# Kernel tuning notes

Measured on AMD Instinct MI355X. Metric: run time of the kernel, lower is better.

Reference implementation:

```python
import jax, jax.numpy as jnp
import numpy as np

EMBED_DIM = 1024
NUM_HEADS = 16
HEAD_DIM = EMBED_DIM // NUM_HEADS


def setup_inputs() -> dict:
    key = jax.random.key(0)
    ks = jax.random.split(key, 9)
    B, T, C = 2, 2048, EMBED_DIM
    s = 1.0 / np.sqrt(C)
    return {
        "x": jax.random.normal(ks[0], (B, T, C), dtype=jnp.float32),
        "Wq": jax.random.normal(ks[1], (C, C), dtype=jnp.float32) * s,
        "bq": jnp.zeros((C,), dtype=jnp.float32),
        "Wk": jax.random.normal(ks[2], (C, C), dtype=jnp.float32) * s,
        "bk": jnp.zeros((C,), dtype=jnp.float32),
        "Wv": jax.random.normal(ks[3], (C, C), dtype=jnp.float32) * s,
        "bv": jnp.zeros((C,), dtype=jnp.float32),
        "Wo": jax.random.normal(ks[4], (C, C), dtype=jnp.float32) * s,
        "bo": jnp.zeros((C,), dtype=jnp.float32),
    }


def reference(x, Wq, bq, Wk, bk, Wv, bv, Wo, bo):
    B, T, C = x.shape
    H, D = NUM_HEADS, HEAD_DIM
    # projections (torch Linear: x @ W.T + b; here W stored as [in,out])
    q = (x @ Wq + bq).reshape(B, T, H, D).transpose(0, 2, 1, 3)  # [B,H,T,D]
    k = (x @ Wk + bk).reshape(B, T, H, D).transpose(0, 2, 1, 3)
    v = (x @ Wv + bv).reshape(B, T, H, D).transpose(0, 2, 1, 3)
    scores = jnp.einsum("bhtd,bhsd->bhts", q, k) / jnp.sqrt(jnp.float32(D))
    causal = jnp.tril(jnp.ones((T, T), dtype=bool))  # keep lower triangle
    scores = jnp.where(causal, scores, -jnp.inf)
    weights = jax.nn.softmax(scores, axis=-1)
    attended = jnp.einsum("bhts,bhsd->bhtd", weights, v)
    attended = attended.transpose(0, 2, 1, 3).reshape(B, T, C)
    return attended @ Wo + bo
```

## Files before the change

kernel.cpp:

```cpp
#include <hip/hip_runtime.h>
#include <math.h>


#define BLOCK 256

typedef __attribute__((ext_vector_type(8))) short bf16x8;
typedef __attribute__((ext_vector_type(4))) float f32x4;
typedef __attribute__((ext_vector_type(16))) float f32x16;

__device__ inline short f2bf(float f) {
  union { float f; unsigned u; } c; c.f = f;
  unsigned u = c.u;
  unsigned r = (u + 0x7fffu + ((u >> 16) & 1u)) >> 16;
  return (short)r;
}


__global__ void cvt_all_kernel(const float* __restrict__ x,
                               const float* __restrict__ Wq, const float* __restrict__ Wk,
                               const float* __restrict__ Wv, const float* __restrict__ Wo,
                               short* __restrict__ xb,
                               short* __restrict__ Wtqkv, short* __restrict__ Wto) {
  __shared__ float tile[32][33];
  __shared__ __align__(16) short xtile[4096];
  int z = blockIdx.z;
  if (z >= 4) {
    int blk = blockIdx.x + (blockIdx.y << 5);
    int rt = blk >> 2, sq = blk & 3;
    int row_l = threadIdx.x >> 4, q = threadIdx.x & 15;
    const float* xr = x + (size_t)(rt * 16 + row_l) * 1024 + sq * 256 + q * 16;
    float4 f0 = *(const float4*)(xr);
    float4 f1 = *(const float4*)(xr + 4);
    float4 f2 = *(const float4*)(xr + 8);
    float4 f3 = *(const float4*)(xr + 12);
    alignas(16) short e0[8], e1[8];
    e0[0] = f2bf(f0.x); e0[1] = f2bf(f0.y); e0[2] = f2bf(f0.z); e0[3] = f2bf(f0.w);
    e0[4] = f2bf(f1.x); e0[5] = f2bf(f1.y); e0[6] = f2bf(f1.z); e0[7] = f2bf(f1.w);
    e1[0] = f2bf(f2.x); e1[1] = f2bf(f2.y); e1[2] = f2bf(f2.z); e1[3] = f2bf(f2.w);
    e1[4] = f2bf(f3.x); e1[5] = f2bf(f3.y); e1[6] = f2bf(f3.z); e1[7] = f2bf(f3.w);
    int c0 = q * 2, c1 = q * 2 + 1;
    *(int4*)&xtile[(c0 * 16 + (row_l ^ (c0 & 15))) * 8] = *(const int4*)e0;
    *(int4*)&xtile[(c1 * 16 + (row_l ^ (c1 & 15))) * 8] = *(const int4*)e1;
    __syncthreads();
    int lc = threadIdx.x & 15, c8x = threadIdx.x >> 4;
#pragma unroll
    for (int hh = 0; hh < 2; hh++) {
      int c8l = c8x + hh * 16;
      int4 v = *(const int4*)&xtile[(c8l * 16 + (lc ^ (c8l & 15))) * 8];
      int s = sq * 4 + (c8l >> 3), c8 = c8l & 7;
      *(int4*)&xb[(size_t)rt * 16384 + s * 1024 + c8 * 128 + lc * 8] = v;
    }
    return;
  }
  const float* W = (z == 0) ? Wq : (z == 1) ? Wk : (z == 2) ? Wv : Wo;
  short* outp = (z == 3) ? Wto : (Wtqkv + (size_t)z * 1024 * 1024);
  int k0 = blockIdx.x * 32, n0 = blockIdx.y * 32;
  int tr = threadIdx.x >> 5, tc = threadIdx.x & 31;
#pragma unroll
  for (int i = 0; i < 4; i++)
    tile[tr + i * 8][tc] = W[(k0 + tr + i * 8) * 1024 + n0 + tc];
  __syncthreads();
#pragma unroll
  for (int i = 0; i < 4; i++)
    outp[(n0 + tr + i * 8) * 1024 + k0 + tc] = f2bf(tile[tc][tr + i * 8]);
}


__global__ __launch_bounds__(BLOCK, 3) void gemm_qkv_kernel(
    const short* __restrict__ A, const short* __restrict__ Wt,
    const float* __restrict__ bq, const float* __restrict__ bk,
    const float* __restrict__ bv,
    short* __restrict__ Qo, short* __restrict__ Ko, short* __restrict__ Vo) {
  const int Kd = 1024;
  const float QSCL = 0.18033688011f;
  int p = blockIdx.x;
  int xcd = p & 7, j = p >> 3;
  int m0 = ((xcd & 3) * 8 + (j & 7)) * 128;
  int n0 = ((xcd >> 2) * 12 + (j >> 3)) * 128;
  int t = threadIdx.x;
  int lane = t & 63, wv = t >> 6;
  int quad = lane >> 4, lc = lane & 15;
  int wy = wv >> 1, wx = wv & 1;
  __shared__ short Bs[128 * 64];
  f32x4 acc[4][4] = {};

  int sr = wv * 32 + (lane >> 3);
  int schk = lane & 7;
  const short* Bb = Wt + (size_t)(n0 + sr) * Kd + schk * 8;
  int wslot = schk ^ (lane >> 3);
  short* wb = &Bs[sr * 64 + wslot * 8];
  const short* Ap = A + (size_t)m0 * 1024;
  int abase = wy * 4 * 16384 + lane * 8;

  bf16x8 sB[4];
#pragma unroll
  for (int i = 0; i < 4; i++)
    sB[i] = *(const bf16x8*)(Bb + (size_t)(i * 8) * Kd);

  int rx = lc & 7;
  for (int step = 0; step < 16; step++) {
#pragma unroll
    for (int i = 0; i < 4; i++)
      *(bf16x8*)(wb + i * 8 * 64) = sB[i];
    asm volatile("s_waitcnt lgkmcnt(0)" ::: "memory");
    __builtin_amdgcn_s_barrier();
    asm volatile("" ::: "memory");
    bf16x8 af2[2][4];
#pragma unroll
    for (int kc2 = 0; kc2 < 2; kc2++)
#pragma unroll
      for (int i = 0; i < 4; i++)
        af2[kc2][i] = *(const bf16x8*)(Ap + (size_t)abase + i * 16384 +
                                       step * 1024 + kc2 * 512);
    if (step + 1 < 16) {
      int koff = (step + 1) * 64;
#pragma unroll
      for (int i = 0; i < 4; i++)
        sB[i] = *(const bf16x8*)(Bb + (size_t)(i * 8) * Kd + koff);
    }
#pragma unroll
    for (int kc = 0; kc < 2; kc++) {
      bf16x8 bf[4];
#pragma unroll
      for (int i = 0; i < 4; i++)
        bf[i] = *(const bf16x8*)&Bs[(wx * 64 + i * 16 + lc) * 64 +
                                    ((kc * 4 + quad) ^ rx) * 8];
#pragma unroll
      for (int mi = 0; mi < 4; mi++)
#pragma unroll
        for (int ni = 0; ni < 4; ni++)
          acc[mi][ni] = __builtin_amdgcn_mfma_f32_16x16x32_bf16(af2[kc][mi], bf[ni], acc[mi][ni], 0, 0, 0);
    }
    asm volatile("s_waitcnt lgkmcnt(0)" ::: "memory");
    __builtin_amdgcn_s_barrier();
    asm volatile("" ::: "memory");
  }
#pragma unroll
  for (int mi = 0; mi < 4; mi++) {
    int row = m0 + wy * 64 + mi * 16 + quad * 4;
#pragma unroll
    for (int ni = 0; ni < 4; ni++) {
      int col = n0 + wx * 64 + ni * 16 + lc;
      int which = col >> 10;
      int hd = col & 1023;
      int h = hd >> 6, d = hd & 63;
      float bb = (which == 0) ? bq[hd] : (which == 1) ? bk[hd] : bv[hd];
      if (which == 2) {
        alignas(8) short pk[4];
#pragma unroll
        for (int r = 0; r < 4; r++) pk[r] = f2bf(acc[mi][ni][r] + bb);
        int b = row >> 11, tt = row & 2047;
        *(int2*)&Vo[((size_t)(b * 16 + h) * 64 + d) * 2048 + tt] = *(const int2*)pk;
      } else {
#pragma unroll
        for (int r = 0; r < 4; r++) {
          int rw = row + r;
          int b = rw >> 11, tt = rw & 2047;
          float val = acc[mi][ni][r] + bb;
          if (which == 0) {
            Qo[((size_t)(b * 16 + h) * 2048 + tt) * 64 + d] = f2bf(val * QSCL);
          } else {
            Ko[((size_t)(b * 16 + h) * 2048 + tt) * 64 + d] = f2bf(val);
          }
        }
      }
    }
  }
}


__global__ __launch_bounds__(BLOCK) void gemm_out_kernel(
    const short* __restrict__ A, const short* __restrict__ Wt,
    const float* __restrict__ bias, float* __restrict__ Out) {
  const int Kd = 1024;
  int m0 = blockIdx.x * 64, n0 = blockIdx.y * 128;
  int t = threadIdx.x;
  int lane = t & 63, wv = t >> 6;
  int quad = lane >> 4, lc = lane & 15;
  int wy = wv >> 1, wx = wv & 1;
  __shared__ short As[64 * 64];
  __shared__ short Bs[128 * 64];
  f32x4 acc[2][4] = {};

  int lr = lane >> 3;
  int schk = lane & 7;
  int wslot = schk ^ lr;
  int srA = wv * 16 + lr;
  int srB = wv * 32 + lr;
  const short* Ab = A + (size_t)(m0 + srA) * Kd + schk * 8;
  const short* Bb = Wt + (size_t)(n0 + srB) * Kd + schk * 8;
  short* wa = &As[srA * 64 + wslot * 8];
  short* wb = &Bs[srB * 64 + wslot * 8];

  bf16x8 sA[2], sB[4];
#pragma unroll
  for (int i = 0; i < 2; i++) sA[i] = *(const bf16x8*)(Ab + (size_t)(i * 8) * Kd);
#pragma unroll
  for (int i = 0; i < 4; i++) sB[i] = *(const bf16x8*)(Bb + (size_t)(i * 8) * Kd);

  int rx = lc & 7;
  for (int step = 0; step < 16; step++) {
#pragma unroll
    for (int i = 0; i < 2; i++) *(bf16x8*)(wa + i * 8 * 64) = sA[i];
#pragma unroll
    for (int i = 0; i < 4; i++) *(bf16x8*)(wb + i * 8 * 64) = sB[i];
    asm volatile("s_waitcnt lgkmcnt(0)" ::: "memory");
    __builtin_amdgcn_s_barrier();
    asm volatile("" ::: "memory");
    if (step + 1 < 16) {
      int koff = (step + 1) * 64;
#pragma unroll
      for (int i = 0; i < 2; i++)
        sA[i] = *(const bf16x8*)(Ab + (size_t)(i * 8) * Kd + koff);
#pragma unroll
      for (int i = 0; i < 4; i++)
        sB[i] = *(const bf16x8*)(Bb + (size_t)(i * 8) * Kd + koff);
    }
#pragma unroll
    for (int kc = 0; kc < 2; kc++) {
      bf16x8 af[2], bf[4];
#pragma unroll
      for (int i = 0; i < 2; i++)
        af[i] = *(const bf16x8*)&As[(wy * 32 + i * 16 + lc) * 64 +
                                    ((kc * 4 + quad) ^ rx) * 8];
#pragma unroll
      for (int i = 0; i < 4; i++)
        bf[i] = *(const bf16x8*)&Bs[(wx * 64 + i * 16 + lc) * 64 +
                                    ((kc * 4 + quad) ^ rx) * 8];
#pragma unroll
      for (int mi = 0; mi < 2; mi++)
#pragma unroll
        for (int ni = 0; ni < 4; ni++)
          acc[mi][ni] = __builtin_amdgcn_mfma_f32_16x16x32_bf16(af[mi], bf[ni], acc[mi][ni], 0, 0, 0);
    }
    asm volatile("s_waitcnt lgkmcnt(0)" ::: "memory");
    __builtin_amdgcn_s_barrier();
    asm volatile("" ::: "memory");
  }
#pragma unroll
  for (int mi = 0; mi < 2; mi++) {
    int row = m0 + wy * 32 + mi * 16 + quad * 4;
#pragma unroll
    for (int ni = 0; ni < 4; ni++) {
      int col = n0 + wx * 64 + ni * 16 + lc;
      float bb = bias[col];
#pragma unroll
      for (int r = 0; r < 4; r++)
        Out[(size_t)(row + r) * 1024 + col] = acc[mi][ni][r] + bb;
    }
  }
}


__global__ __launch_bounds__(BLOCK, 2) void attn_kernel(
    const short* __restrict__ Q, const short* __restrict__ K,
    const short* __restrict__ Vt, short* __restrict__ Oa) {
  int p = blockIdx.x;
  int bh = ((p & 7) << 2) | ((p >> 3) & 3);
  int pair = p >> 5;
  int t = threadIdx.x;
  int lane = t & 63, w = t >> 6;
  int qh = w & 1, kh = w >> 1;
  int ln = lane & 31, lh = lane >> 5;
  const short* Qb = Q + (size_t)bh * 2048 * 64;
  const short* Kb = K + (size_t)bh * 2048 * 64;
  const short* Vg = Vt + (size_t)bh * 64 * 2048;
  int b = bh >> 4, h = bh & 15;

  __shared__ short Kt[64 * 64];
  __shared__ short Vs[64 * 64];
  __shared__ __align__(16) short Ps[4][32 * 72];
  __shared__ float lx[2][64];
  short* Pw = Ps[w];

  int srow = t >> 3;
  int schk = t & 7;
  int wslot = (schk ^ (srow & 7)) * 8;
  const float M2 = 14.5f;
  int xk = ln & 7;

  for (int sp = 0; sp < 2; sp++) {
    int s = sp ? (31 - pair) : pair;
    int q0 = s * 64;
    int q0w = q0 + qh * 32;
    int qmaxw = q0w + 31;
    int ntiles = s + 1;

    bf16x8 qf[4];
#pragma unroll
    for (int c = 0; c < 4; c++)
      qf[c] = *(const bf16x8*)&Qb[(size_t)(q0w + ln) * 64 + c * 16 + lh * 8];

    f32x16 O0 = {}, O1 = {};
    float lsum = 0.f;

    bf16x8 sK[2], sV[2];
#pragma unroll
    for (int i = 0; i < 2; i++) {
      int r = i * 32 + srow;
      sK[i] = *(const bf16x8*)&Kb[(size_t)r * 64 + schk * 8];
      sV[i] = *(const bf16x8*)&Vg[(size_t)r * 2048 + schk * 8];
    }
    for (int kt = 0; kt < ntiles; kt++) {
#pragma unroll
      for (int i = 0; i < 2; i++) {
        int r = i * 32 + srow;
        *(bf16x8*)&Kt[r * 64 + wslot] = sK[i];
        *(bf16x8*)&Vs[r * 64 + wslot] = sV[i];
      }
      asm volatile("s_waitcnt lgkmcnt(0)" ::: "memory");
      __builtin_amdgcn_s_barrier();
      asm volatile("" ::: "memory");
      if (kt + 1 < ntiles) {
        int kb2 = (kt + 1) * 64;
#pragma unroll
        for (int i = 0; i < 2; i++) {
          int r = i * 32 + srow;
          sK[i] = *(const bf16x8*)&Kb[(size_t)(kb2 + r) * 64 + schk * 8];
          sV[i] = *(const bf16x8*)&Vg[(size_t)r * 2048 + kb2 + schk * 8];
        }
      }
      int grpbase = kt * 64 + kh * 32;
      if (grpbase <= qmaxw) {
        f32x16 S = {};
#pragma unroll
        for (int c = 0; c < 4; c++) {
          int ch = c * 2 + lh;
          bf16x8 kf = *(const bf16x8*)&Kt[(kh * 32 + ln) * 64 + (ch ^ xk) * 8];
          S = __builtin_amdgcn_mfma_f32_32x32x16_bf16(kf, qf[c], S, 0, 0, 0);
        }
        if (kt == ntiles - 1) {
          int qg = q0w + ln;
#pragma unroll
          for (int reg = 0; reg < 16; reg++) {
            int key = grpbase + (reg & 3) + 8 * (reg >> 2) + 4 * lh;
            if (key > qg) S[reg] = -3.0e38f;
          }
        }
#pragma unroll
        for (int g = 0; g < 4; g++) {
          unsigned u[4];
#pragma unroll
          for (int i = 0; i < 4; i++) {
            union { float f; unsigned v; } cc;
            cc.f = __builtin_amdgcn_exp2f(S[g * 4 + i] - M2);
            lsum += cc.f;
            u[i] = cc.v + 0x8000u;
          }
          int2 pk;
          pk.x = (int)__builtin_amdgcn_perm(u[1], u[0], 0x07060302);
          pk.y = (int)__builtin_amdgcn_perm(u[3], u[2], 0x07060302);
          *(int2*)&Pw[ln * 72 + g * 8 + lh * 4] = pk;
        }
#pragma unroll
        for (int c2 = 0; c2 < 2; c2++) {
          bf16x8 pf = *(const bf16x8*)&Pw[ln * 72 + c2 * 16 + lh * 8];
          int ch = kh * 4 + c2 * 2 + lh;
          bf16x8 v0 = *(const bf16x8*)&Vs[ln * 64 + (ch ^ xk) * 8];
          bf16x8 v1 = *(const bf16x8*)&Vs[(32 + ln) * 64 + (ch ^ xk) * 8];
          O0 = __builtin_amdgcn_mfma_f32_32x32x16_bf16(v0, pf, O0, 0, 0, 0);
          O1 = __builtin_amdgcn_mfma_f32_32x32x16_bf16(v1, pf, O1, 0, 0, 0);
        }
      }
      asm volatile("s_waitcnt lgkmcnt(0)" ::: "memory");
      __builtin_amdgcn_s_barrier();
      asm volatile("" ::: "memory");
    }

    float* ob = (float*)&Ps[0][0];
    if (kh == 1) {
      float* obw = ob + qh * 2048;
#pragma unroll
      for (int dh = 0; dh < 2; dh++)
#pragma unroll
        for (int reg = 0; reg < 16; reg++)
          obw[((dh * 16 + reg) * 2 + lh) * 32 + ln] = dh ? O1[reg] : O0[reg];
      lx[qh][lane] = lsum;
    }
    __syncthreads();
    if (kh == 0) {
      float* obw = ob + qh * 2048;
#pragma unroll
      for (int reg = 0; reg < 16; reg++) {
        O0[reg] += obw[((0 * 16 + reg) * 2 + lh) * 32 + ln];
        O1[reg] += obw[((1 * 16 + reg) * 2 + lh) * 32 + ln];
      }
      float lt = lsum + lx[qh][lane];
      lt += __shfl_xor(lt, 32, 64);
      float inv = 1.0f / lt;
      size_t rowbase = (size_t)(b * 2048 + q0w + ln) * 1024 + h * 64;
#pragma unroll
      for (int dh = 0; dh < 2; dh++)
#pragma unroll
        for (int g = 0; g < 4; g++) {
          alignas(8) short pk[4];
#pragma unroll
          for (int i = 0; i < 4; i++) {
            float v = dh ? O1[g * 4 + i] : O0[g * 4 + i];
            pk[i] = f2bf(v * inv);
          }
          *(int2*)&Oa[rowbase + dh * 32 + g * 8 + lh * 4] = *(const int2*)pk;
        }
    }
  }
}


extern "C" void kernel_launch(void* const* d_in, const int* in_sizes, int n_in,
                              void* d_out, int out_size, void* d_ws, size_t ws_size,
                              hipStream_t stream) {
  const float* x = (const float*)d_in[0];
  const float* Wq = (const float*)d_in[1];
  const float* bq = (const float*)d_in[2];
  const float* Wk = (const float*)d_in[3];
  const float* bk = (const float*)d_in[4];
  const float* Wv = (const float*)d_in[5];
  const float* bv = (const float*)d_in[6];
  const float* Wo = (const float*)d_in[7];
  const float* bo = (const float*)d_in[8];
  char* ws = (char*)d_ws;
  const size_t MB = 1024 * 1024;
  short* xb = (short*)(ws);
  short* Wtqkv = (short*)(ws + 8 * MB);
  short* Wto = (short*)(ws + 14 * MB);
  short* Qb = (short*)(ws + 17 * MB);
  short* Kb = (short*)(ws + 25 * MB);
  short* Vb = (short*)(ws + 33 * MB);
  short* Att = (short*)(ws + 41 * MB);
  float* out = (float*)d_out;

  cvt_all_kernel<<<dim3(32, 32, 5), BLOCK, 0, stream>>>(x, Wq, Wk, Wv, Wo, xb, Wtqkv, Wto);
  gemm_qkv_kernel<<<dim3(768), BLOCK, 0, stream>>>(xb, Wtqkv, bq, bk, bv, Qb, Kb, Vb);
  attn_kernel<<<512, BLOCK, 0, stream>>>(Qb, Kb, Vb, Att);
  gemm_out_kernel<<<dim3(64, 8), BLOCK, 0, stream>>>(Att, Wto, bo, out);
}
```

Before: 175.1 us.

## Assign each wave its own 32 query rows over 128-row blocks, drop key-split reduction

The attention kernel previously had each block handle two 64-row query tiles (a balanced pair). Within a tile, waves split the key dimension in halves and merged partial outputs through shared memory. Now each block handles one 128-row query tile, with the 16 tiles assigned largest-first. Each of the four waves owns 32 query rows and walks all keys itself, which removes the cross-wave O/lsum reduction and its extra barrier. In exchange, per-block work is unbalanced across the grid, and waves with early query rows sit idle on later key tiles because of the causal mask.

Result: slower. 179.7 us (+2.6%).

```diff
diff --git a/kernel.cpp b/kernel.cpp
--- a/kernel.cpp
+++ b/kernel.cpp
@@ -257,10 +257,10 @@
     const short* __restrict__ Vt, short* __restrict__ Oa) {
   int p = blockIdx.x;
   int bh = ((p & 7) << 2) | ((p >> 3) & 3);
-  int pair = p >> 5;
+  int g = p >> 5;
+  int s = (g < 8) ? (15 - g) : (g - 8);
   int t = threadIdx.x;
   int lane = t & 63, w = t >> 6;
-  int qh = w & 1, kh = w >> 1;
   int ln = lane & 31, lh = lane >> 5;
   const short* Qb = Q + (size_t)bh * 2048 * 64;
   const short* Kb = K + (size_t)bh * 2048 * 64;
@@ -270,7 +270,6 @@
   __shared__ short Kt[64 * 64];
   __shared__ short Vs[64 * 64];
   __shared__ __align__(16) short Ps[4][32 * 72];
-  __shared__ float lx[2][64];
   short* Pw = Ps[w];
 
   int srow = t >> 3;
@@ -279,57 +278,56 @@
   const float M2 = 14.5f;
   int xk = ln & 7;
 
-  for (int sp = 0; sp < 2; sp++) {
-    int s = sp ? (31 - pair) : pair;
-    int q0 = s * 64;
-    int q0w = q0 + qh * 32;
-    int qmaxw = q0w + 31;
-    int ntiles = s + 1;
-
-    bf16x8 qf[4];
-#pragma unroll
-    for (int c = 0; c < 4; c++)
-      qf[c] = *(const bf16x8*)&Qb[(size_t)(q0w + ln) * 64 + c * 16 + lh * 8];
-
-    f32x16 O0 = {}, O1 = {};
-    float lsum = 0.f;
-
-    bf16x8 sK[2], sV[2];
+  int q0w = s * 128 + w * 32;
+  int qmaxw = q0w + 31;
+  int ntiles = 2 * (s + 1);
+
+  bf16x8 qf[4];
+#pragma unroll
+  for (int c = 0; c < 4; c++)
+    qf[c] = *(const bf16x8*)&Qb[(size_t)(q0w + ln) * 64 + c * 16 + lh * 8];
+
+  f32x16 O0 = {}, O1 = {};
+  float lsum = 0.f;
+
+  bf16x8 sK[2], sV[2];
+#pragma unroll
+  for (int i = 0; i < 2; i++) {
+    int r = i * 32 + srow;
+    sK[i] = *(const bf16x8*)&Kb[(size_t)r * 64 + schk * 8];
+    sV[i] = *(const bf16x8*)&Vg[(size_t)r * 2048 + schk * 8];
+  }
+  for (int kt = 0; kt < ntiles; kt++) {
 #pragma unroll
     for (int i = 0; i < 2; i++) {
       int r = i * 32 + srow;
-      sK[i] = *(const bf16x8*)&Kb[(size_t)r * 64 + schk * 8];
-      sV[i] = *(const bf16x8*)&Vg[(size_t)r * 2048 + schk * 8];
-    }
-    for (int kt = 0; kt < ntiles; kt++) {
+      *(bf16x8*)&Kt[r * 64 + wslot] = sK[i];
+      *(bf16x8*)&Vs[r * 64 + wslot] = sV[i];
+    }
+    asm volatile("s_waitcnt lgkmcnt(0)" ::: "memory");
+    __builtin_amdgcn_s_barrier();
+    asm volatile("" ::: "memory");
+    if (kt + 1 < ntiles) {
+      int kb2 = (kt + 1) * 64;
 #pragma unroll
       for (int i = 0; i < 2; i++) {
         int r = i * 32 + srow;
-        *(bf16x8*)&Kt[r * 64 + wslot] = sK[i];
-        *(bf16x8*)&Vs[r * 64 + wslot] = sV[i];
+        sK[i] = *(const bf16x8*)&Kb[(size_t)(kb2 + r) * 64 + schk * 8];
+        sV[i] = *(const bf16x8*)&Vg[(size_t)r * 2048 + kb2 + schk * 8];
       }
-      asm volatile("s_waitcnt lgkmcnt(0)" ::: "memory");
-      __builtin_amdgcn_s_barrier();
-      asm volatile("" ::: "memory");
-      if (kt + 1 < ntiles) {
-        int kb2 = (kt + 1) * 64;
-#pragma unroll
-        for (int i = 0; i < 2; i++) {
-          int r = i * 32 + srow;
-          sK[i] = *(const bf16x8*)&Kb[(size_t)(kb2 + r) * 64 + schk * 8];
-          sV[i] = *(const bf16x8*)&Vg[(size_t)r * 2048 + kb2 + schk * 8];
-        }
-      }
-      int grpbase = kt * 64 + kh * 32;
+    }
+#pragma unroll
+    for (int kg = 0; kg < 2; kg++) {
+      int grpbase = kt * 64 + kg * 32;
       if (grpbase <= qmaxw) {
         f32x16 S = {};
 #pragma unroll
         for (int c = 0; c < 4; c++) {
           int ch = c * 2 + lh;
-          bf16x8 kf = *(const bf16x8*)&Kt[(kh * 32 + ln) * 64 + (ch ^ xk) * 8];
+          bf16x8 kf = *(const bf16x8*)&Kt[(kg * 32 + ln) * 64 + (ch ^ xk) * 8];
           S = __builtin_amdgcn_mfma_f32_32x32x16_bf16(kf, qf[c], S, 0, 0, 0);
         }
-        if (kt == ntiles - 1) {
+        if (grpbase + 31 > q0w) {
           int qg = q0w + ln;
 #pragma unroll
           for (int reg = 0; reg < 16; reg++) {
@@ -338,71 +336,54 @@
           }
         }
 #pragma unroll
-        for (int g = 0; g < 4; g++) {
+        for (int g4 = 0; g4 < 4; g4++) {
           unsigned u[4];
+          float e[4];
 #pragma unroll
           for (int i = 0; i < 4; i++) {
             union { float f; unsigned v; } cc;
-            cc.f = __builtin_amdgcn_exp2f(S[g * 4 + i] - M2);
-            lsum += cc.f;
+            cc.f = __builtin_amdgcn_exp2f(S[g4 * 4 + i] - M2);
+            e[i] = cc.f;
             u[i] = cc.v + 0x8000u;
           }
+          lsum += (e[0] + e[1]) + (e[2] + e[3]);
           int2 pk;
           pk.x = (int)__builtin_amdgcn_perm(u[1], u[0], 0x07060302);
           pk.y = (int)__builtin_amdgcn_perm(u[3], u[2], 0x07060302);
-          *(int2*)&Pw[ln * 72 + g * 8 + lh * 4] = pk;
+          *(int2*)&Pw[ln * 72 + kg * 32 + g4 * 8 + lh * 4] = pk;
         }
 #pragma unroll
-        for (int c2 = 0; c2 < 2; c2++) {
-          bf16x8 pf = *(const bf16x8*)&Pw[ln * 72 + c2 * 16 + lh * 8];
-          int ch = kh * 4 + c2 * 2 + lh;
+        for (int cc = 0; cc < 2; cc++) {
+          bf16x8 pf = *(const bf16x8*)&Pw[ln * 72 + kg * 32 + cc * 16 + lh * 8];
+          int ch = kg * 4 + cc * 2 + lh;
           bf16x8 v0 = *(const bf16x8*)&Vs[ln * 64 + (ch ^ xk) * 8];
           bf16x8 v1 = *(const bf16x8*)&Vs[(32 + ln) * 64 + (ch ^ xk) * 8];
           O0 = __builtin_amdgcn_mfma_f32_32x32x16_bf16(v0, pf, O0, 0, 0, 0);
           O1 = __builtin_amdgcn_mfma_f32_32x32x16_bf16(v1, pf, O1, 0, 0, 0);
         }
       }
-      asm volatile("s_waitcnt lgkmcnt(0)" ::: "memory");
-      __builtin_amdgcn_s_barrier();
-      asm volatile("" ::: "memory");
-    }
-
-    float* ob = (float*)&Ps[0][0];
-    if (kh == 1) {
-      float* obw = ob + qh * 2048;
-#pragma unroll
-      for (int dh = 0; dh < 2; dh++)
-#pragma unroll
-        for (int reg = 0; reg < 16; reg++)
-          obw[((dh * 16 + reg) * 2 + lh) * 32 + ln] = dh ? O1[reg] : O0[reg];
-      lx[qh][lane] = lsum;
-    }
-    __syncthreads();
-    if (kh == 0) {
-      float* obw = ob + qh * 2048;
-#pragma unroll
-      for (int reg = 0; reg < 16; reg++) {
-        O0[reg] += obw[((0 * 16 + reg) * 2 + lh) * 32 + ln];
-        O1[reg] += obw[((1 * 16 + reg) * 2 + lh) * 32 + ln];
+    }
+    asm volatile("s_waitcnt lgkmcnt(0)" ::: "memory");
+    __builtin_amdgcn_s_barrier();
+    asm volatile("" ::: "memory");
+  }
+
+  float lt = lsum;
+  lt += __shfl_xor(lt, 32, 64);
+  float inv = 1.0f / lt;
+  size_t rowbase = (size_t)(b * 2048 + q0w + ln) * 1024 + h * 64;
+#pragma unroll
+  for (int dh = 0; dh < 2; dh++)
+#pragma unroll
+    for (int g4 = 0; g4 < 4; g4++) {
+      alignas(8) short pk[4];
+#pragma unroll
+      for (int i = 0; i < 4; i++) {
+        float v = dh ? O1[g4 * 4 + i] : O0[g4 * 4 + i];
+        pk[i] = f2bf(v * inv);
       }
-      float lt = lsum + lx[qh][lane];
-      lt += __shfl_xor(lt, 32, 64);
-      float inv = 1.0f / lt;
-      size_t rowbase = (size_t)(b * 2048 + q0w + ln) * 1024 + h * 64;
-#pragma unroll
-      for (int dh = 0; dh < 2; dh++)
-#pragma unroll
-        for (int g = 0; g < 4; g++) {
-          alignas(8) short pk[4];
-#pragma unroll
-          for (int i = 0; i < 4; i++) {
-            float v = dh ? O1[g * 4 + i] : O0[g * 4 + i];
-            pk[i] = f2bf(v * inv);
-          }
-          *(int2*)&Oa[rowbase + dh * 32 + g * 8 + lh * 4] = *(const int2*)pk;
-        }
-    }
-  }
+      *(int2*)&Oa[rowbase + dh * 32 + g4 * 8 + lh * 4] = *(const int2*)pk;
+    }
 }
 
 
```
